# Kernel tuning notes

Measured on AMD Instinct MI355X. Metric: run time of the kernel, lower is better.

Reference implementation:

```python
import jax, jax.numpy as jnp
import numpy as np
import math

B, SQ, SKV, H = 8, 1024, 1024, 1024
NH, HD = 16, 64  # num_attention_heads, attention_head_size


def setup_inputs() -> dict:
    key = jax.random.key(0)
    ks = jax.random.split(key, 6)
    s = 1.0 / math.sqrt(H)
    return {
        "hidden_states": jax.random.normal(ks[0], (B, SQ, H), jnp.float32),
        "keyvalue_states": jax.random.normal(ks[1], (B, SKV, H), jnp.float32),
        "attention_mask": jnp.zeros((B, 1, 1, SKV), jnp.float32),
        "Wq": jax.random.normal(ks[2], (H, H), jnp.float32) * s,
        "bq": jnp.zeros((H,), jnp.float32),
        "Wk": jax.random.normal(ks[3], (H, H), jnp.float32) * s,
        "bk": jnp.zeros((H,), jnp.float32),
        "Wv": jax.random.normal(ks[4], (H, H), jnp.float32) * s,
        "bv": jnp.zeros((H,), jnp.float32),
    }


def _split_heads(x):
    # [B, S, H] -> [B, NH, S, HD]
    b, s, _ = x.shape
    return x.reshape(b, s, NH, HD).transpose(0, 2, 1, 3)


def reference(hidden_states, keyvalue_states, attention_mask, Wq, bq, Wk, bk, Wv, bv):
    q = _split_heads(hidden_states @ Wq.T + bq)     # [B, NH, SQ, HD]
    k = _split_heads(keyvalue_states @ Wk.T + bk)   # [B, NH, SKV, HD]
    v = _split_heads(keyvalue_states @ Wv.T + bv)   # [B, NH, SKV, HD]
    scores = jnp.einsum("bhqd,bhkd->bhqk", q, k) / math.sqrt(HD)
    scores = scores + attention_mask                 # additive mask broadcast
    probs = jax.nn.softmax(scores, axis=-1)          # dropout = identity (eval)
    ctx = jnp.einsum("bhqk,bhkd->bhqd", probs, v)
    ctx = ctx.transpose(0, 2, 1, 3).reshape(hidden_states.shape[0], -1, NH * HD)
    return ctx
```

## Files before the change

### kernel.cpp

```cpp
#include <hip/hip_runtime.h>
#include <hip/hip_bf16.h>


typedef __attribute__((ext_vector_type(8))) short short8;
typedef __attribute__((ext_vector_type(4))) short short4v;
typedef __attribute__((ext_vector_type(4))) float f32x4;
typedef __attribute__((ext_vector_type(2))) float f32x2;
typedef __attribute__((ext_vector_type(16))) float f32x16;
typedef __attribute__((ext_vector_type(2))) unsigned uint2v;
typedef __attribute__((ext_vector_type(4))) int int4v;

#define AS1(p) ((const __attribute__((address_space(1))) void*)(p))
#define AS3(p) ((__attribute__((address_space(3))) void*)(p))

__device__ inline short f2bs(float x) {
    __hip_bfloat16 h = __float2bfloat16(x);
    return *reinterpret_cast<short*>(&h);
}

__global__ __launch_bounds__(256) void cvt_bf16(
    const float* __restrict__ s0, const float* __restrict__ s1,
    const float* __restrict__ s2, const float* __restrict__ s3,
    const float* __restrict__ s4,
    short* __restrict__ d0, short* __restrict__ d1,
    short* __restrict__ d2, short* __restrict__ d3, short* __restrict__ d4)
{
    const float* s; short* d; int n4;
    switch (blockIdx.y) {
        case 0: s = s0; d = d0; n4 = 2097152; break;
        case 1: s = s1; d = d1; n4 = 2097152; break;
        case 2: s = s2; d = d2; n4 = 262144;  break;
        case 3: s = s3; d = d3; n4 = 262144;  break;
        default: s = s4; d = d4; n4 = 262144; break;
    }
    for (int i = blockIdx.x * 256 + threadIdx.x; i < n4; i += gridDim.x * 256) {
        float4 v = ((const float4*)s)[i];
        short4v o;
        o.x = f2bs(v.x); o.y = f2bs(v.y); o.z = f2bs(v.z); o.w = f2bs(v.w);
        ((short4v*)d)[i] = o;
    }
}


__device__ inline void stage8(const short* __restrict__ A,
                              const short* __restrict__ W,
                              short* As, short* Bs,
                              int t, int m0, int n0, int k0)
{
    #pragma unroll
    for (int i = 0; i < 4; ++i) {
        int c = i * 512 + t;
        int row = c >> 3;
        int gc = (c & 7) ^ (row & 7);
        __builtin_amdgcn_global_load_lds(
            AS1(&A[(size_t)(m0 + row) * 1024 + k0 + gc * 8]), AS3(&As[c * 8]), 16, 0, 0);
    }
    #pragma unroll
    for (int i = 0; i < 4; ++i) {
        int c = i * 512 + t;
        int row = c >> 3;
        int gc = (c & 7) ^ (row & 7);
        __builtin_amdgcn_global_load_lds(
            AS1(&W[(size_t)(n0 + row) * 1024 + k0 + gc * 8]), AS3(&Bs[c * 8]), 16, 0, 0);
    }
}

__global__ __launch_bounds__(512, 2) void qkv_gemm(
    const short* __restrict__ hsb, const short* __restrict__ kvb,
    const short* __restrict__ wqb, const short* __restrict__ wkb,
    const short* __restrict__ wvb,
    const float* __restrict__ bq, const float* __restrict__ bk,
    const float* __restrict__ bv,
    short* __restrict__ qo, short* __restrict__ ko, short* __restrict__ vo)
{
    const short* A; const short* W; const float* bias; short* dst;
    int z = blockIdx.z;
    if (z == 0)      { A = hsb; W = wqb; bias = bq; dst = qo; }
    else if (z == 1) { A = kvb; W = wkb; bias = bk; dst = ko; }
    else             { A = kvb; W = wvb; bias = bv; dst = vo; }

    __shared__ __align__(16) short As[2][256 * 64];
    __shared__ __align__(16) short Bs[2][256 * 64];

    const int t = threadIdx.x;
    const int lane = t & 63;
    const int wid = t >> 6;
    const int lane31 = lane & 31;
    const int hi = lane >> 5;
    const int wr = wid >> 2;
    const int wc = wid & 3;
    const int m0 = blockIdx.x * 256;
    const int n0 = blockIdx.y * 256;

    f32x16 acc[4][2] = {};

    stage8(A, W, &As[0][0], &Bs[0][0], t, m0, n0, 0);
    stage8(A, W, &As[1][0], &Bs[1][0], t, m0, n0, 64);

    for (int kt = 0; kt < 16; ++kt) {
        if (kt == 15) asm volatile("s_waitcnt vmcnt(0)" ::: "memory");
        else          asm volatile("s_waitcnt vmcnt(8)" ::: "memory");
        __builtin_amdgcn_s_barrier();

        const short* as_ = &As[kt & 1][0];
        const short* bs_ = &Bs[kt & 1][0];

        #pragma unroll
        for (int kc = 0; kc < 4; ++kc) {
            short8 af[4], bf[2];
            #pragma unroll
            for (int mt = 0; mt < 4; ++mt) {
                int rr = wr * 128 + mt * 32 + lane31;
                af[mt] = *(const short8*)&as_[rr * 64 + (((kc * 2 + hi)) ^ (rr & 7)) * 8];
            }
            #pragma unroll
            for (int nt = 0; nt < 2; ++nt) {
                int rn = wc * 64 + nt * 32 + lane31;
                bf[nt] = *(const short8*)&bs_[rn * 64 + (((kc * 2 + hi)) ^ (rn & 7)) * 8];
            }
            __builtin_amdgcn_s_barrier();
            asm volatile("s_waitcnt lgkmcnt(0)" ::: "memory");
            __builtin_amdgcn_sched_barrier(0);
            __builtin_amdgcn_s_setprio(1);
            #pragma unroll
            for (int mt = 0; mt < 4; ++mt)
                #pragma unroll
                for (int nt = 0; nt < 2; ++nt)
                    acc[mt][nt] = __builtin_amdgcn_mfma_f32_32x32x16_bf16(
                        af[mt], bf[nt], acc[mt][nt], 0, 0, 0);
            __builtin_amdgcn_s_setprio(0);
            __builtin_amdgcn_s_barrier();
        }

        __builtin_amdgcn_sched_barrier(0);
        if (kt < 14)
            stage8(A, W, &As[kt & 1][0], &Bs[kt & 1][0], t, m0, n0, (kt + 2) * 64);
        __builtin_amdgcn_sched_barrier(0);
    }

    if (z != 2) {
        #pragma unroll
        for (int nt = 0; nt < 2; ++nt) {
            int col = n0 + wc * 64 + nt * 32 + lane31;
            float bb = bias[col];
            int h = col >> 6, d = col & 63;
            #pragma unroll
            for (int mt = 0; mt < 4; ++mt) {
                #pragma unroll
                for (int rg = 0; rg < 4; ++rg) {
                    int m = m0 + wr * 128 + mt * 32 + rg * 8 + hi * 4;
                    int b = m >> 10, s = m & 1023;
                    size_t base = (size_t)((b * 16 + h) * 1024 + s) * 64 + d;
                    #pragma unroll
                    for (int r = 0; r < 4; ++r)
                        dst[base + (size_t)r * 64] = f2bs(acc[mt][nt][rg * 4 + r] + bb);
                }
            }
        }
    } else {
        #pragma unroll
        for (int nt = 0; nt < 2; ++nt) {
            int col = n0 + wc * 64 + nt * 32 + lane31;
            float bb = bias[col];
            int h = col >> 6, d = col & 63;
            #pragma unroll
            for (int mt = 0; mt < 4; ++mt) {
                #pragma unroll
                for (int rg = 0; rg < 4; ++rg) {
                    int m = m0 + wr * 128 + mt * 32 + rg * 8 + hi * 4;
                    int b = m >> 10, s = m & 1023;
                    short4v pk;
                    pk.x = f2bs(acc[mt][nt][rg * 4 + 0] + bb);
                    pk.y = f2bs(acc[mt][nt][rg * 4 + 1] + bb);
                    pk.z = f2bs(acc[mt][nt][rg * 4 + 2] + bb);
                    pk.w = f2bs(acc[mt][nt][rg * 4 + 3] + bb);
                    *(short4v*)&dst[(size_t)((b * 16 + h) * 64 + d) * 1024 + s] = pk;
                }
            }
        }
    }
}

#define EXPC 0.18033688011112042f
#define LOG2E 1.4426950408889634f

__device__ inline uint2v half_swap(unsigned c, unsigned d, int hi) {
#if __has_builtin(__builtin_amdgcn_permlane32_swap)
    return __builtin_amdgcn_permlane32_swap(c, d, false, false);
#else
    unsigned send = hi ? c : d;
    unsigned recv = (unsigned)__shfl_xor((int)send, 32, 64);
    uint2v r;
    r.x = hi ? recv : c;
    r.y = hi ? d : recv;
    return r;
#endif
}

__device__ inline float fast_exp2(float x) {
#if __has_builtin(__builtin_amdgcn_exp2f)
    return __builtin_amdgcn_exp2f(x);
#else
    float r;
    asm("v_exp_f32 %0, %1" : "=v"(r) : "v"(x));
    return r;
#endif
}

__device__ inline unsigned cvt_pk_bf16(float a, float b) {
    unsigned r;
    asm("v_cvt_pk_bf16_f32 %0, %1, %2" : "=v"(r) : "v"(a), "v"(b));
    return r;
}

__global__ __launch_bounds__(256, 4) void attn(
    const short* __restrict__ q, const short* __restrict__ k,
    const short* __restrict__ vt, const float* __restrict__ mask,
    float* __restrict__ out)
{
    __shared__ __align__(16) short Ks[2][64 * 64];
    __shared__ __align__(16) short Vs[2][64 * 64];
    __shared__ __align__(16) float Ems[1024];

    const int t = threadIdx.x;
    const int lane = t & 63;
    const int wq = t >> 6;
    const int lane31 = lane & 31;
    const int hi = lane >> 5;

    const int id = blockIdx.x;
    const int bh = (id >> 6) * 8 + (id & 7);
    const int qt = (id >> 3) & 7;
    const int b = bh >> 4, h = bh & 15;

    const short* qbase = q + (size_t)(bh * 1024 + qt * 128) * 64;
    const short* kbase = k + (size_t)bh * 1024 * 64;
    const short* vbase = vt + (size_t)bh * 64 * 1024;

    {
        float4 mv = ((const float4*)(mask + b * 1024))[t];
        float4 o4;
        o4.x = mv.x * LOG2E; o4.y = mv.y * LOG2E;
        o4.z = mv.z * LOG2E; o4.w = mv.w * LOG2E;
        *(float4*)&Ems[t * 4] = o4;
    }

    short8 qf[4];
    #pragma unroll
    for (int kc = 0; kc < 4; ++kc)
        qf[kc] = *(const short8*)&qbase[(size_t)(wq * 32 + lane31) * 64 + kc * 16 + hi * 8];

    #pragma unroll
    for (int i = 0; i < 2; ++i) {
        int c = i * 256 + t;
        int row = c >> 3;
        int gc = (c & 7) ^ (row & 7);
        __builtin_amdgcn_global_load_lds(AS1(kbase + (size_t)row * 64 + gc * 8),
                                         AS3(&Ks[0][c * 8]), 16, 0, 0);
        __builtin_amdgcn_global_load_lds(AS1(vbase + (size_t)row * 1024 + gc * 8),
                                         AS3(&Vs[0][c * 8]), 16, 0, 0);
    }

    f32x16 o_acc[2] = {};
    f32x2 lacc = {0.f, 0.f};

    for (int kt = 0; kt < 16; ++kt) {
        __syncthreads();
        if (kt < 15) {
            int kv1 = (kt + 1) * 64;
            int nb = (kt + 1) & 1;
            #pragma unroll
            for (int i = 0; i < 2; ++i) {
                int c = i * 256 + t;
                int row = c >> 3;
                int gc = (c & 7) ^ (row & 7);
                __builtin_amdgcn_global_load_lds(
                    AS1(kbase + (size_t)(kv1 + row) * 64 + gc * 8),
                    AS3(&Ks[nb][c * 8]), 16, 0, 0);
                __builtin_amdgcn_global_load_lds(
                    AS1(vbase + (size_t)row * 1024 + kv1 + gc * 8),
                    AS3(&Vs[nb][c * 8]), 16, 0, 0);
            }
        }
        const short* ks_ = Ks[kt & 1];
        const short* vs_ = Vs[kt & 1];
        const int kv0 = kt * 64;

        f32x16 sacc[2] = {};
        #pragma unroll
        for (int kc = 0; kc < 4; ++kc) {
            #pragma unroll
            for (int mt = 0; mt < 2; ++mt) {
                int rr = mt * 32 + lane31;
                short8 ak = *(short8*)&ks_[rr * 64 + ((kc * 2 + hi) ^ (rr & 7)) * 8];
                sacc[mt] = __builtin_amdgcn_mfma_f32_32x32x16_bf16(ak, qf[kc], sacc[mt], 0, 0, 0);
            }
        }

        unsigned pk[2][4][2];
        #pragma unroll
        for (int mt = 0; mt < 2; ++mt) {
            #pragma unroll
            for (int rg = 0; rg < 4; ++rg) {
                int kvl = mt * 32 + rg * 8 + hi * 4;
                f32x4 mk = *(const f32x4*)&Ems[kv0 + kvl];
                f32x4 sv;
                sv.x = sacc[mt][rg * 4 + 0];
                sv.y = sacc[mt][rg * 4 + 1];
                sv.z = sacc[mt][rg * 4 + 2];
                sv.w = sacc[mt][rg * 4 + 3];
                f32x4 ev = sv * EXPC + mk;
                float p0 = fast_exp2(ev.x);
                float p1 = fast_exp2(ev.y);
                float p2 = fast_exp2(ev.z);
                float p3 = fast_exp2(ev.w);
                f32x2 pa; pa.x = p0; pa.y = p2;
                f32x2 pb; pb.x = p1; pb.y = p3;
                lacc += pa + pb;
                pk[mt][rg][0] = cvt_pk_bf16(p0, p1);
                pk[mt][rg][1] = cvt_pk_bf16(p2, p3);
            }
        }

        #pragma unroll
        for (int kc = 0; kc < 4; ++kc) {
            const int mt = kc >> 1, glo = (kc & 1) * 2;
            uint2v s0 = half_swap(pk[mt][glo][0], pk[mt][glo + 1][0], hi);
            uint2v s1 = half_swap(pk[mt][glo][1], pk[mt][glo + 1][1], hi);
            int4v fr; fr.x = (int)s0.x; fr.y = (int)s1.x; fr.z = (int)s0.y; fr.w = (int)s1.y;
            short8 ap = *(short8*)&fr;
            #pragma unroll
            for (int nt = 0; nt < 2; ++nt) {
                int rv = nt * 32 + lane31;
                short8 bv_ = *(short8*)&vs_[rv * 64 + ((kc * 2 + hi) ^ (rv & 7)) * 8];
                o_acc[nt] = __builtin_amdgcn_mfma_f32_32x32x16_bf16(ap, bv_, o_acc[nt], 0, 0, 0);
            }
        }
    }

    float l_sum = lacc.x + lacc.y;
    l_sum += __shfl_xor(l_sum, 32, 64);
    float invl = 1.f / l_sum;

    #pragma unroll
    for (int rg = 0; rg < 4; ++rg) {
        #pragma unroll
        for (int r = 0; r < 4; ++r) {
            int qrow_l = rg * 8 + hi * 4 + r;
            float lv = __shfl(invl, qrow_l, 64);
            int qrow = qt * 128 + wq * 32 + qrow_l;
            size_t base = (size_t)(b * 1024 + qrow) * 1024 + h * 64;
            #pragma unroll
            for (int nt = 0; nt < 2; ++nt)
                out[base + nt * 32 + lane31] = o_acc[nt][rg * 4 + r] * lv;
        }
    }
}

extern "C" void kernel_launch(void* const* d_in, const int* in_sizes, int n_in,
                              void* d_out, int out_size, void* d_ws, size_t ws_size,
                              hipStream_t stream) {
    const float* hs   = (const float*)d_in[0];
    const float* kvs  = (const float*)d_in[1];
    const float* mask = (const float*)d_in[2];
    const float* Wq   = (const float*)d_in[3];
    const float* bq   = (const float*)d_in[4];
    const float* Wk   = (const float*)d_in[5];
    const float* bk   = (const float*)d_in[6];
    const float* Wv   = (const float*)d_in[7];
    const float* bv   = (const float*)d_in[8];
    float* outp = (float*)d_out;

    const size_t big = (size_t)8 * 1024 * 1024;
    const size_t wsz = (size_t)1024 * 1024;
    short* q_ws  = (short*)d_ws;
    short* k_ws  = q_ws  + big;
    short* vt_ws = k_ws  + big;
    short* hsb   = vt_ws + big;
    short* kvb   = hsb   + big;
    short* wqb   = kvb   + big;
    short* wkb   = wqb   + wsz;
    short* wvb   = wkb   + wsz;

    cvt_bf16<<<dim3(1024, 5), 256, 0, stream>>>(hs, kvs, Wq, Wk, Wv,
                                                hsb, kvb, wqb, wkb, wvb);
    qkv_gemm<<<dim3(32, 4, 3), 512, 0, stream>>>(hsb, kvb, wqb, wkb, wvb,
                                                 bq, bk, bv, q_ws, k_ws, vt_ws);
    attn<<<dim3(1024), 256, 0, stream>>>(q_ws, k_ws, vt_ws, mask, outp);
}
```

Measured before the change: 260.1 us.

## Triple-buffer QKV GEMM with 256x128 tiles and interleaved async loads

The QKV projection GEMM now uses 256x128 output tiles instead of 256x256, which doubles the grid to 768 blocks. Its LDS staging goes from two buffers to three. Global-to-LDS loads for stage k+2 are split and issued between the LDS fragment reads of the current stage instead of after the compute loop, so memory traffic overlaps the MFMA work. The smaller N tile lowers per-block accumulator registers, but the launch bound drops to one block per SIMD group, and each block reloads the A tile from global twice as often overall.

```diff
diff --git a/kernel.cpp b/kernel.cpp
--- a/kernel.cpp
+++ b/kernel.cpp
@@ -41,31 +41,7 @@
     }
 }
 
-
-__device__ inline void stage8(const short* __restrict__ A,
-                              const short* __restrict__ W,
-                              short* As, short* Bs,
-                              int t, int m0, int n0, int k0)
-{
-    #pragma unroll
-    for (int i = 0; i < 4; ++i) {
-        int c = i * 512 + t;
-        int row = c >> 3;
-        int gc = (c & 7) ^ (row & 7);
-        __builtin_amdgcn_global_load_lds(
-            AS1(&A[(size_t)(m0 + row) * 1024 + k0 + gc * 8]), AS3(&As[c * 8]), 16, 0, 0);
-    }
-    #pragma unroll
-    for (int i = 0; i < 4; ++i) {
-        int c = i * 512 + t;
-        int row = c >> 3;
-        int gc = (c & 7) ^ (row & 7);
-        __builtin_amdgcn_global_load_lds(
-            AS1(&W[(size_t)(n0 + row) * 1024 + k0 + gc * 8]), AS3(&Bs[c * 8]), 16, 0, 0);
-    }
-}
-
-__global__ __launch_bounds__(512, 2) void qkv_gemm(
+__global__ __launch_bounds__(512, 1) void qkv_gemm(
     const short* __restrict__ hsb, const short* __restrict__ kvb,
     const short* __restrict__ wqb, const short* __restrict__ wkb,
     const short* __restrict__ wvb,
@@ -79,8 +55,8 @@
     else if (z == 1) { A = kvb; W = wkb; bias = bk; dst = ko; }
     else             { A = kvb; W = wvb; bias = bv; dst = vo; }
 
-    __shared__ __align__(16) short As[2][256 * 64];
-    __shared__ __align__(16) short Bs[2][256 * 64];
+    __shared__ __align__(16) short As[3][256 * 64];
+    __shared__ __align__(16) short Bs[3][128 * 64];
 
     const int t = threadIdx.x;
     const int lane = t & 63;
@@ -90,92 +66,112 @@
     const int wr = wid >> 2;
     const int wc = wid & 3;
     const int m0 = blockIdx.x * 256;
-    const int n0 = blockIdx.y * 256;
-
-    f32x16 acc[4][2] = {};
-
-    stage8(A, W, &As[0][0], &Bs[0][0], t, m0, n0, 0);
-    stage8(A, W, &As[1][0], &Bs[1][0], t, m0, n0, 64);
-
+    const int n0 = blockIdx.y * 128;
+
+    f32x16 acc[4] = {};
+
+    auto STAGE_A2 = [&](int buf, int k0, int i0) {
+        #pragma unroll
+        for (int i = i0; i < i0 + 2; ++i) {
+            int c = i * 512 + t;
+            int row = c >> 3;
+            int gc = (c & 7) ^ (row & 7);
+            __builtin_amdgcn_global_load_lds(
+                AS1(&A[(size_t)(m0 + row) * 1024 + k0 + gc * 8]),
+                AS3(&As[buf][c * 8]), 16, 0, 0);
+        }
+    };
+    auto STAGE_B2 = [&](int buf, int k0) {
+        #pragma unroll
+        for (int i = 0; i < 2; ++i) {
+            int c = i * 512 + t;
+            int row = c >> 3;
+            int gc = (c & 7) ^ (row & 7);
+            __builtin_amdgcn_global_load_lds(
+                AS1(&W[(size_t)(n0 + row) * 1024 + k0 + gc * 8]),
+                AS3(&Bs[buf][c * 8]), 16, 0, 0);
+        }
+    };
+
+    STAGE_A2(0, 0, 0);  STAGE_A2(0, 0, 2);  STAGE_B2(0, 0);
+    STAGE_A2(1, 64, 0); STAGE_A2(1, 64, 2); STAGE_B2(1, 64);
+
+    int cur = 0;
     for (int kt = 0; kt < 16; ++kt) {
         if (kt == 15) asm volatile("s_waitcnt vmcnt(0)" ::: "memory");
-        else          asm volatile("s_waitcnt vmcnt(8)" ::: "memory");
+        else          asm volatile("s_waitcnt vmcnt(6)" ::: "memory");
         __builtin_amdgcn_s_barrier();
 
-        const short* as_ = &As[kt & 1][0];
-        const short* bs_ = &Bs[kt & 1][0];
-
-        #pragma unroll
-        for (int kc = 0; kc < 4; ++kc) {
-            short8 af[4], bf[2];
-            #pragma unroll
-            for (int mt = 0; mt < 4; ++mt) {
-                int rr = wr * 128 + mt * 32 + lane31;
-                af[mt] = *(const short8*)&as_[rr * 64 + (((kc * 2 + hi)) ^ (rr & 7)) * 8];
-            }
-            #pragma unroll
-            for (int nt = 0; nt < 2; ++nt) {
-                int rn = wc * 64 + nt * 32 + lane31;
-                bf[nt] = *(const short8*)&bs_[rn * 64 + (((kc * 2 + hi)) ^ (rn & 7)) * 8];
+        const short* as_ = &As[cur][0];
+        const short* bs_ = &Bs[cur][0];
+        int stg = cur + 2; if (stg >= 3) stg -= 3;
+        const int k2 = (kt + 2) * 64;
+        const bool do_stage = (kt < 14);
+
+        #pragma unroll
+        for (int p = 0; p < 2; ++p) {
+            short8 af[2][4], bf[2];
+            #pragma unroll
+            for (int qq = 0; qq < 2; ++qq) {
+                const int kc = p * 2 + qq;
+                #pragma unroll
+                for (int mt = 0; mt < 4; ++mt) {
+                    int rr = wr * 128 + mt * 32 + lane31;
+                    af[qq][mt] = *(const short8*)&as_[rr * 64 + ((kc * 2 + hi) ^ (rr & 7)) * 8];
+                }
+                int rn = wc * 32 + lane31;
+                bf[qq] = *(const short8*)&bs_[rn * 64 + ((kc * 2 + hi) ^ (rn & 7)) * 8];
+            }
+            if (do_stage) {
+                if (p == 0) { STAGE_A2(stg, k2, 0); STAGE_B2(stg, k2); }
+                else        { STAGE_A2(stg, k2, 2); }
             }
             __builtin_amdgcn_s_barrier();
             asm volatile("s_waitcnt lgkmcnt(0)" ::: "memory");
             __builtin_amdgcn_sched_barrier(0);
             __builtin_amdgcn_s_setprio(1);
             #pragma unroll
-            for (int mt = 0; mt < 4; ++mt)
+            for (int qq = 0; qq < 2; ++qq)
                 #pragma unroll
-                for (int nt = 0; nt < 2; ++nt)
-                    acc[mt][nt] = __builtin_amdgcn_mfma_f32_32x32x16_bf16(
-                        af[mt], bf[nt], acc[mt][nt], 0, 0, 0);
+                for (int mt = 0; mt < 4; ++mt)
+                    acc[mt] = __builtin_amdgcn_mfma_f32_32x32x16_bf16(
+                        af[qq][mt], bf[qq], acc[mt], 0, 0, 0);
             __builtin_amdgcn_s_setprio(0);
             __builtin_amdgcn_s_barrier();
         }
 
-        __builtin_amdgcn_sched_barrier(0);
-        if (kt < 14)
-            stage8(A, W, &As[kt & 1][0], &Bs[kt & 1][0], t, m0, n0, (kt + 2) * 64);
-        __builtin_amdgcn_sched_barrier(0);
-    }
-
+        cur = (cur == 2) ? 0 : cur + 1;
+    }
+
+    const int col = n0 + wc * 32 + lane31;
+    const float bb = bias[col];
+    const int h = col >> 6, d = col & 63;
     if (z != 2) {
         #pragma unroll
-        for (int nt = 0; nt < 2; ++nt) {
-            int col = n0 + wc * 64 + nt * 32 + lane31;
-            float bb = bias[col];
-            int h = col >> 6, d = col & 63;
-            #pragma unroll
-            for (int mt = 0; mt < 4; ++mt) {
+        for (int mt = 0; mt < 4; ++mt) {
+            #pragma unroll
+            for (int rg = 0; rg < 4; ++rg) {
+                int m = m0 + wr * 128 + mt * 32 + rg * 8 + hi * 4;
+                int b = m >> 10, s = m & 1023;
+                size_t base = (size_t)((b * 16 + h) * 1024 + s) * 64 + d;
                 #pragma unroll
-                for (int rg = 0; rg < 4; ++rg) {
-                    int m = m0 + wr * 128 + mt * 32 + rg * 8 + hi * 4;
-                    int b = m >> 10, s = m & 1023;
-                    size_t base = (size_t)((b * 16 + h) * 1024 + s) * 64 + d;
-                    #pragma unroll
-                    for (int r = 0; r < 4; ++r)
-                        dst[base + (size_t)r * 64] = f2bs(acc[mt][nt][rg * 4 + r] + bb);
-                }
+                for (int r = 0; r < 4; ++r)
+                    dst[base + (size_t)r * 64] = f2bs(acc[mt][rg * 4 + r] + bb);
             }
         }
     } else {
         #pragma unroll
-        for (int nt = 0; nt < 2; ++nt) {
-            int col = n0 + wc * 64 + nt * 32 + lane31;
-            float bb = bias[col];
-            int h = col >> 6, d = col & 63;
-            #pragma unroll
-            for (int mt = 0; mt < 4; ++mt) {
-                #pragma unroll
-                for (int rg = 0; rg < 4; ++rg) {
-                    int m = m0 + wr * 128 + mt * 32 + rg * 8 + hi * 4;
-                    int b = m >> 10, s = m & 1023;
-                    short4v pk;
-                    pk.x = f2bs(acc[mt][nt][rg * 4 + 0] + bb);
-                    pk.y = f2bs(acc[mt][nt][rg * 4 + 1] + bb);
-                    pk.z = f2bs(acc[mt][nt][rg * 4 + 2] + bb);
-                    pk.w = f2bs(acc[mt][nt][rg * 4 + 3] + bb);
-                    *(short4v*)&dst[(size_t)((b * 16 + h) * 64 + d) * 1024 + s] = pk;
-                }
+        for (int mt = 0; mt < 4; ++mt) {
+            #pragma unroll
+            for (int rg = 0; rg < 4; ++rg) {
+                int m = m0 + wr * 128 + mt * 32 + rg * 8 + hi * 4;
+                int b = m >> 10, s = m & 1023;
+                short4v pk;
+                pk.x = f2bs(acc[mt][rg * 4 + 0] + bb);
+                pk.y = f2bs(acc[mt][rg * 4 + 1] + bb);
+                pk.z = f2bs(acc[mt][rg * 4 + 2] + bb);
+                pk.w = f2bs(acc[mt][rg * 4 + 3] + bb);
+                *(short4v*)&dst[(size_t)((b * 16 + h) * 64 + d) * 1024 + s] = pk;
             }
         }
     }
@@ -384,7 +380,7 @@
 
     cvt_bf16<<<dim3(1024, 5), 256, 0, stream>>>(hs, kvs, Wq, Wk, Wv,
                                                 hsb, kvb, wqb, wkb, wvb);
-    qkv_gemm<<<dim3(32, 4, 3), 512, 0, stream>>>(hsb, kvb, wqb, wkb, wvb,
+    qkv_gemm<<<dim3(32, 8, 3), 512, 0, stream>>>(hsb, kvb, wqb, wkb, wvb,
                                                  bq, bk, bv, q_ws, k_ws, vt_ws);
     attn<<<dim3(1024), 256, 0, stream>>>(q_ws, k_ws, vt_ws, mask, outp);
 }
```

New measurement: 240.3 us. 1.08x faster.
